# Kernel tuning notes

Hardware: AMD Instinct MI355X
Metric: run time of the kernel (lower is better)

## Reference

```python
import jax, jax.numpy as jnp
import numpy as np


def setup_inputs() -> dict:
    key = jax.random.key(0)
    k1, k2, k3, k4 = jax.random.split(key, 4)
    B, L, D = 16, 2048, 128
    return {
        "query": jax.random.normal(k1, (B, L, D), dtype=jnp.float32),
        "key": jax.random.normal(k2, (B, L, D), dtype=jnp.float32),
        "value": jax.random.normal(k3, (B, L, D), dtype=jnp.float32),
        "mask": jax.random.randint(k4, (B, L, L), 0, 2, dtype=jnp.int32),
    }


def reference(query, key, value, mask):
    # scores: [B, L_q, L_k], scaled by sqrt(D_q)
    scale = 1.0 / jnp.sqrt(jnp.asarray(query.shape[-1], dtype=query.dtype))
    scores = jnp.einsum("bqd,bkd->bqk", query, key) * scale
    NEG = jnp.asarray(-1e9, dtype=scores.dtype)
    scores = jnp.where(mask == 0, NEG, scores)
    p_attn = jax.nn.softmax(scores, axis=-1)
    context = jnp.einsum("bqk,bkd->bqd", p_attn, value)
    return (context, p_attn)
```

## Files before the change

kernel.cpp:

```cpp
#include <hip/hip_runtime.h>
#include <hip/hip_bf16.h>
#include <hip/hip_fp16.h>

#define BB 16
#define LL 2048
#define DD 128
#define SCALE 0.08838834764831845f
#define CEXP 12.0f
#define NT 32

typedef _Float16 f16x8 __attribute__((ext_vector_type(8)));
typedef float f32x16 __attribute__((ext_vector_type(16)));

#define MFMA32(a,b,c) __builtin_amdgcn_mfma_f32_32x32x16_f16((a),(b),(c),0,0,0)

#define OFF_KB   0
#define OFF_VB   65536
#define OFF_PB   131072
#define OFF_RED  147456
#define LDS_MAIN 148480

#define WAITVM(N)  asm volatile("s_waitcnt vmcnt(" #N ")" ::: "memory")
#define MEMFENCE   asm volatile("" ::: "memory")
#define SB0        __builtin_amdgcn_sched_barrier(0)

__device__ __forceinline__ f16x8 as_f16x8(uint4 v){
  union { uint4 u; f16x8 h; } x; x.u = v; return x.h;
}
__device__ __forceinline__ unsigned pkf16(float a, float b){
  __half ha = __float2half_rn(a), hb = __float2half_rn(b);
  return (unsigned)__half_as_ushort(ha) | ((unsigned)__half_as_ushort(hb) << 16);
}
__device__ __forceinline__ unsigned pkrtz(float a, float b){
  union { decltype(__builtin_amdgcn_cvt_pkrtz(0.f, 0.f)) h; unsigned u; } x;
  x.h = __builtin_amdgcn_cvt_pkrtz(a, b);
  return x.u;
}
__device__ __forceinline__ void stage16(const unsigned char* g, char* l){
  __builtin_amdgcn_global_load_lds(
      (const __attribute__((address_space(1))) void*)g,
      (__attribute__((address_space(3))) void*)l, 16, 0, 0);
}
__device__ __forceinline__ void stage2(const unsigned char* g, char* l, int soff){
  stage16(g + soff, l + soff);
  stage16(g + soff + 1024, l + soff + 1024);
}

__global__ __launch_bounds__(256) void prep_img(
    const float* __restrict__ K, const float* __restrict__ V,
    unsigned char* __restrict__ kimg, unsigned char* __restrict__ vimg)
{
  __shared__ float t[32][65];
  const int bid = blockIdx.x, tid = threadIdx.x;
  if (bid < 2048) {
    const int G = bid*256 + tid;
    const int b = G >> 15;
    const int k = (G >> 4) & 2047;
    const int gd = G & 15;
    const float* src = K + ((size_t)b*LL + k)*DD + gd*8;
    float4 f0 = *(const float4*)(src);
    float4 f1 = *(const float4*)(src + 4);
    uint4 o;
    o.x = pkf16(f0.x, f0.y); o.y = pkf16(f0.z, f0.w);
    o.z = pkf16(f1.x, f1.y); o.w = pkf16(f1.z, f1.w);
    const size_t base = ((size_t)b*NT + (k>>6))*16384;
    *(uint4*)(kimg + base + (k&63)*256 + ((gd*16) ^ ((k&15)<<4))) = o;
  } else {
    const int t2 = bid - 2048;
    const int b = t2 >> 7;
    const int rem = t2 & 127;
    const int kt = rem >> 2, dt = rem & 3;
    const int k0 = kt*64, d0 = dt*32;
    const int kl = tid >> 2, dq = (tid & 3)*8;
    const float* src = V + ((size_t)b*LL + k0 + kl)*DD + d0 + dq;
    float4 f0 = *(const float4*)(src);
    float4 f1 = *(const float4*)(src + 4);
    t[dq+0][kl] = f0.x; t[dq+1][kl] = f0.y; t[dq+2][kl] = f0.z; t[dq+3][kl] = f0.w;
    t[dq+4][kl] = f1.x; t[dq+5][kl] = f1.y; t[dq+6][kl] = f1.z; t[dq+7][kl] = f1.w;
    __syncthreads();
    const int dl = tid >> 3, kg = tid & 7;
    const int d = d0 + dl;
    uint4 o;
    o.x = pkf16(t[dl][kg*8+0], t[dl][kg*8+1]);
    o.y = pkf16(t[dl][kg*8+2], t[dl][kg*8+3]);
    o.z = pkf16(t[dl][kg*8+4], t[dl][kg*8+5]);
    o.w = pkf16(t[dl][kg*8+6], t[dl][kg*8+7]);
    const size_t base = ((size_t)b*NT + kt)*16384;
    *(uint4*)(vimg + base + d*128 + ((kg*16) ^ ((d&7)<<4))) = o;
  }
}

#define QKCOMPUTE(BUFIDX) \
  const char* kb = KB + (BUFIDX)*16384 + krow*256; \
  f32x16 aA, aB; \
  _Pragma("unroll") for (int i=0;i<16;++i){aA[i]=0.f;aB[i]=0.f;} \
  _Pragma("unroll") for (int s=0;s<4;++s){ \
    uint4 af = *(const uint4*)(kb + (((s*2+hi)*16) ^ kswz)); \
    aA = MFMA32(as_f16x8(af), as_f16x8(qf[s]), aA); } \
  _Pragma("unroll") for (int s=4;s<8;++s){ \
    uint4 af = *(const uint4*)(kb + (((s*2+hi)*16) ^ kswz)); \
    aB = MFMA32(as_f16x8(af), as_f16x8(qf[s]), aB); }

#define P1BODY(RR, WN) do { \
  WAITVM(WN); \
  __builtin_amdgcn_s_barrier(); \
  MEMFENCE; \
  int4 t0, t1, t2, t3; \
  { const int* mp2 = Mrow + (((RR)+2)&31)*64 + moff; \
    t0 = *(const int4*)(mp2);    t1 = *(const int4*)(mp2+8); \
    t2 = *(const int4*)(mp2+16); t3 = *(const int4*)(mp2+24); } \
  SB0; \
  stage2(KIMG + imgb + (size_t)(((RR)+3)&31)*16384, KB + (((RR)+3)&3)*16384, soff); \
  SB0; \
  QKCOMPUTE((RR)&3); \
  const unsigned w16 = (cm0.x?0x1u:0u) | (cm0.y?0x2u:0u) | (cm0.z?0x4u:0u) | (cm0.w?0x8u:0u) \
                     | (cm1.x?0x100u:0u) | (cm1.y?0x200u:0u) | (cm1.z?0x400u:0u) | (cm1.w?0x800u:0u) \
                     | (cm2.x?0x10000u:0u) | (cm2.y?0x20000u:0u) | (cm2.z?0x40000u:0u) | (cm2.w?0x80000u:0u) \
                     | (cm3.x?0x1000000u:0u) | (cm3.y?0x2000000u:0u) | (cm3.z?0x4000000u:0u) | (cm3.w?0x8000000u:0u); \
  { const unsigned pw = __shfl_xor(w16, 32); \
    if (l < 32) BMst[(RR)*2] = w16 | (pw << 4); } \
  _Pragma("unroll") for (int i=0;i<16;++i){ \
    const float sv = ((w16>>((i&3)+8*(i>>2)))&1u) ? fmaf(aA[i]+aB[i], SCALE, -CEXP) : -1.0e9f; \
    psum[i&3] += __expf(sv); } \
  cm0=n10; cm1=n11; cm2=n12; cm3=n13; \
  n10=t0; n11=t1; n12=t2; n13=t3; \
} while(0)

#define P2BODY(RR, NTOK) do { \
  WAITVM(NTOK); \
  __builtin_amdgcn_s_barrier(); \
  MEMFENCE; \
  const unsigned bn2 = BMl[2*(((RR)+2)&31)]; \
  SB0; \
  stage2(KIMG + imgb + (size_t)(((RR)+3)&31)*16384, KB + (((RR)+3)&3)*16384, soff); \
  stage2(VIMG + imgb + (size_t)(((RR)+3)&31)*16384, VB + (((RR)+3)&3)*16384, soff); \
  SB0; \
  QKCOMPUTE((RR)&3); \
  const unsigned bwh = bcur >> (4*hi); \
  float pv[16]; \
  _Pragma("unroll") for (int i=0;i<16;++i){ \
    const float sv = ((bwh>>((i&3)+8*(i>>2)))&1u) ? fmaf(aA[i]+aB[i], SCALE, -CEXP) : -1.0e9f; \
    pv[i] = __expf(sv) * inv; } \
  { float* pr = Prow + (size_t)(RR)*64 + sub*32 + hi*4; \
    float4 o; \
    o.x=pv[0];  o.y=pv[1];  o.z=pv[2];  o.w=pv[3];  *(float4*)(pr)    = o; \
    o.x=pv[4];  o.y=pv[5];  o.z=pv[6];  o.w=pv[7];  *(float4*)(pr+8)  = o; \
    o.x=pv[8];  o.y=pv[9];  o.z=pv[10]; o.w=pv[11]; *(float4*)(pr+16) = o; \
    o.x=pv[12]; o.y=pv[13]; o.z=pv[14]; o.w=pv[15]; *(float4*)(pr+24) = o; } \
  SB0; \
  { char* pb = PB + p*4096 + sub*2048; \
    uint2 u; \
    u.x = pkrtz(pv[0],pv[1]);   u.y = pkrtz(pv[2],pv[3]);   *(uint2*)(pb + c*16 + hi*8) = u; \
    u.x = pkrtz(pv[4],pv[5]);   u.y = pkrtz(pv[6],pv[7]);   *(uint2*)(pb + (c+32)*16 + hi*8) = u; \
    u.x = pkrtz(pv[8],pv[9]);   u.y = pkrtz(pv[10],pv[11]); *(uint2*)(pb + 1024 + c*16 + hi*8) = u; \
    u.x = pkrtz(pv[12],pv[13]); u.y = pkrtz(pv[14],pv[15]); *(uint2*)(pb + 1024 + (c+32)*16 + hi*8) = u; } \
  asm volatile("s_waitcnt lgkmcnt(0)" ::: "memory"); \
  __builtin_amdgcn_s_barrier(); \
  MEMFENCE; \
  _Pragma("unroll") for (int s2=0;s2<2;++s2){ \
    _Pragma("unroll") for (int k2=0;k2<2;++k2){ \
      const uint4 afr = *(const uint4*)(PB + p*4096 + s2*2048 + k2*1024 + l*16); \
      const int gix = s2*4 + k2*2 + hi; \
      const int d0v = sub*64 + c; \
      const uint4 b0 = *(const uint4*)(VB + ((RR)&3)*16384 + d0v*128 + ((gix*16) ^ ((d0v&7)<<4))); \
      ctx0 = MFMA32(as_f16x8(afr), as_f16x8(b0), ctx0); \
      const int d1v = sub*64 + 32 + c; \
      const uint4 b1 = *(const uint4*)(VB + ((RR)&3)*16384 + d1v*128 + ((gix*16) ^ ((d1v&7)<<4))); \
      ctx1 = MFMA32(as_f16x8(afr), as_f16x8(b1), ctx1); } } \
  bcur = bn1; bn1 = bn2; \
} while(0)

__global__ __launch_bounds__(512) void attn_main(
    const float* __restrict__ Q, const int* __restrict__ M,
    unsigned int* __restrict__ BM,
    const unsigned char* __restrict__ KIMG, const unsigned char* __restrict__ VIMG,
    float* __restrict__ ctxout, float* __restrict__ pout)
{
  extern __shared__ char lds[];
  char* KB = lds + OFF_KB;
  char* VB = lds + OFF_VB;
  char* PB = lds + OFF_PB;
  float* RED = (float*)(lds + OFF_RED);

  const int tid = threadIdx.x;
  const int w = tid >> 6, l = tid & 63;
  const int c = l & 31, hi = l >> 5;
  const int p = w >> 1, sub = w & 1;

  const int bid = blockIdx.x;
  const int xcd = bid & 7, jj = bid >> 3;
  const int b = xcd*2 + (jj >> 4);
  const int q0 = (jj & 15) * 128;
  const int qrow = q0 + p*32 + c;

  uint4 qf[8];
  const float* qp0 = Q + ((size_t)b*LL + qrow)*DD;
#pragma unroll
  for (int s = 0; s < 8; ++s) {
    const float4 f0 = *(const float4*)(qp0 + s*16 + hi*8);
    const float4 f1 = *(const float4*)(qp0 + s*16 + hi*8 + 4);
    uint4 qv;
    qv.x = pkf16(f0.x, f0.y); qv.y = pkf16(f0.z, f0.w);
    qv.z = pkf16(f1.x, f1.y); qv.w = pkf16(f1.z, f1.w);
    qf[s] = qv;
  }

  const size_t imgb = ((size_t)b * NT) * 16384;
  const int soff = w*2048 + l*16;
  const int* Mrow = M + ((size_t)b*LL + qrow)*LL;
  const int moff = sub*32 + hi*4;
  unsigned int* BMst = BM + ((size_t)b*LL + qrow)*64 + sub;
  const unsigned int* BMl = BMst;
  const int krow = sub*32 + c;
  const int kswz = (c & 15) << 4;

  int4 cm0, cm1, cm2, cm3, n10, n11, n12, n13;
  stage2(KIMG + imgb + 0*16384, KB + 0*16384, soff); SB0;
  { const int* mp = Mrow + moff;
    cm0 = *(const int4*)(mp);    cm1 = *(const int4*)(mp+8);
    cm2 = *(const int4*)(mp+16); cm3 = *(const int4*)(mp+24); } SB0;
  stage2(KIMG + imgb + 1*16384, KB + 1*16384, soff); SB0;
  { const int* mp = Mrow + 64 + moff;
    n10 = *(const int4*)(mp);    n11 = *(const int4*)(mp+8);
    n12 = *(const int4*)(mp+16); n13 = *(const int4*)(mp+24); } SB0;
  stage2(KIMG + imgb + 2*16384, KB + 2*16384, soff); SB0;

  float psum[4] = {0.f, 0.f, 0.f, 0.f};
  P1BODY(0, 8);
  P1BODY(1, 9);
#pragma unroll 1
  for (int r = 2; r < 32; ++r) {
    P1BODY(r, 10);
  }
  float sum = (psum[0] + psum[1]) + (psum[2] + psum[3]);
  sum += __shfl_xor(sum, 32);
  __syncthreads();
  if (l < 32) RED[(p*2+sub)*32 + c] = sum;
  __syncthreads();
  float tot = RED[(p*2+sub)*32 + c] + RED[(p*2+(1-sub))*32 + c];
  tot = fmaxf(tot, 1e-35f);
  const float inv = 1.0f / tot;
  __syncthreads();

  stage2(KIMG + imgb + 0*16384, KB + 0*16384, soff);
  stage2(VIMG + imgb + 0*16384, VB + 0*16384, soff); SB0;
  unsigned bcur = BMl[0]; SB0;
  stage2(KIMG + imgb + 1*16384, KB + 1*16384, soff);
  stage2(VIMG + imgb + 1*16384, VB + 1*16384, soff); SB0;
  unsigned bn1 = BMl[2]; SB0;
  stage2(KIMG + imgb + 2*16384, KB + 2*16384, soff);
  stage2(VIMG + imgb + 2*16384, VB + 2*16384, soff); SB0;

  f32x16 ctx0, ctx1;
#pragma unroll
  for (int i = 0; i < 16; ++i) { ctx0[i] = 0.f; ctx1[i] = 0.f; }
  float* Prow = pout + ((size_t)b*LL + qrow)*LL;

  P2BODY(0, 10);
  P2BODY(1, 14);
  P2BODY(2, 18);
#pragma unroll 1
  for (int r = 3; r < 32; ++r) {
    P2BODY(r, 22);
  }

#pragma unroll
  for (int reg = 0; reg < 16; ++reg) {
    const int q = q0 + p*32 + (reg&3) + 8*(reg>>2) + 4*hi;
    float* cr = ctxout + ((size_t)b*LL + q)*DD;
    cr[sub*64 + c]      = ctx0[reg];
    cr[sub*64 + 32 + c] = ctx1[reg];
  }
}

__global__ __launch_bounds__(256) void attn_naive(
    const float* __restrict__ Q, const float* __restrict__ K,
    const float* __restrict__ V, const int* __restrict__ M,
    float* __restrict__ ctx, float* __restrict__ pout)
{
  const int b = blockIdx.x >> 11;
  const int q = blockIdx.x & (LL-1);
  __shared__ float s[LL];
  __shared__ float red[256];
  const int tid = threadIdx.x;
  const float* qp = Q + ((size_t)b*LL + q)*DD;
  for (int kk = tid; kk < LL; kk += 256) {
    const float* kp = K + ((size_t)b*LL + kk)*DD;
    float a = 0.f;
    for (int d = 0; d < DD; ++d) a += qp[d]*kp[d];
    s[kk] = M[((size_t)b*LL + q)*LL + kk] ? a*SCALE : -1e9f;
  }
  __syncthreads();
  float mx = -3e38f;
  for (int kk = tid; kk < LL; kk += 256) mx = fmaxf(mx, s[kk]);
  red[tid] = mx; __syncthreads();
  for (int o = 128; o >= 1; o >>= 1) {
    if (tid < o) red[tid] = fmaxf(red[tid], red[tid+o]);
    __syncthreads();
  }
  const float mrow = red[0]; __syncthreads();
  float sm = 0.f;
  for (int kk = tid; kk < LL; kk += 256) { float e = __expf(s[kk]-mrow); s[kk] = e; sm += e; }
  red[tid] = sm; __syncthreads();
  for (int o = 128; o >= 1; o >>= 1) {
    if (tid < o) red[tid] += red[tid+o];
    __syncthreads();
  }
  const float inv = 1.0f / red[0]; __syncthreads();
  float* prow = pout + ((size_t)b*LL + q)*LL;
  for (int kk = tid; kk < LL; kk += 256) { s[kk] *= inv; prow[kk] = s[kk]; }
  __syncthreads();
  if (tid < DD) {
    float a = 0.f;
    for (int kk = 0; kk < LL; ++kk) a += s[kk]*V[((size_t)b*LL + kk)*DD + tid];
    ctx[((size_t)b*LL + q)*DD + tid] = a;
  }
}

extern "C" void kernel_launch(void* const* d_in, const int* in_sizes, int n_in,
                              void* d_out, int out_size, void* d_ws, size_t ws_size,
                              hipStream_t stream) {
  (void)in_sizes; (void)n_in; (void)out_size;
  const float* Q = (const float*)d_in[0];
  const float* K = (const float*)d_in[1];
  const float* V = (const float*)d_in[2];
  const int*   M = (const int*)d_in[3];
  float* ctx  = (float*)d_out;
  float* pout = ctx + (size_t)BB*LL*DD;
  const size_t IMG = (size_t)BB*NT*16384;
  const size_t NBM = (size_t)BB*LL*(LL/32);
  const size_t WS_NEED = IMG*2 + NBM*4;
  if (ws_size >= WS_NEED) {
    unsigned char* kimg = (unsigned char*)d_ws;
    unsigned char* vimg = kimg + IMG;
    unsigned int*  bmw  = (unsigned int*)(vimg + IMG);
    hipFuncSetAttribute(reinterpret_cast<const void*>(attn_main),
                        hipFuncAttributeMaxDynamicSharedMemorySize, LDS_MAIN);
    prep_img<<<4096, 256, 0, stream>>>(K, V, kimg, vimg);
    attn_main<<<256, 512, LDS_MAIN, stream>>>(Q, M, bmw, kimg, vimg, ctx, pout);
  } else {
    attn_naive<<<BB*LL, 256, 0, stream>>>(Q, K, V, M, ctx, pout);
  }
}
```

Measured before the change: 218.2 us.

## Stage mask tiles into LDS via async global_load_lds with swizzled layout

Pass 1 no longer loads mask int4s directly into registers two steps ahead. Each block now cooperatively stages 128x64 mask tiles into a double-buffered LDS region with async direct-to-LDS loads and an XOR swizzle, then reads them back from LDS. The aim is coalesced, fully-line mask reads, lower register pressure, and a simpler vmcnt pipeline. The cost is more LDS traffic. The mask buffer also reuses the V buffer region, so phase 1 must finish with it before phase 2 stages V.

```diff
diff --git a/kernel.cpp b/kernel.cpp
--- a/kernel.cpp
+++ b/kernel.cpp
@@ -15,10 +15,11 @@
 #define MFMA32(a,b,c) __builtin_amdgcn_mfma_f32_32x32x16_f16((a),(b),(c),0,0,0)
 
 #define OFF_KB   0
-#define OFF_VB   65536
+#define OFF_MB   65536
 #define OFF_PB   131072
 #define OFF_RED  147456
 #define LDS_MAIN 148480
+#define OFF_VB   65536
 
 #define WAITVM(N)  asm volatile("s_waitcnt vmcnt(" #N ")" ::: "memory")
 #define MEMFENCE   asm volatile("" ::: "memory")
@@ -44,6 +45,12 @@
 __device__ __forceinline__ void stage2(const unsigned char* g, char* l, int soff){
   stage16(g + soff, l + soff);
   stage16(g + soff + 1024, l + soff + 1024);
+}
+__device__ __forceinline__ void mstage(const unsigned char* msrc, char* mdst, int roff){
+  stage16(msrc + roff,          mdst);
+  stage16(msrc + roff + 262144, mdst + 8192);
+  stage16(msrc + roff + 524288, mdst + 16384);
+  stage16(msrc + roff + 786432, mdst + 24576);
 }
 
 __global__ __launch_bounds__(256) void prep_img(
@@ -105,32 +112,32 @@
   WAITVM(WN); \
   __builtin_amdgcn_s_barrier(); \
   MEMFENCE; \
-  int4 t0, t1, t2, t3; \
-  { const int* mp2 = Mrow + (((RR)+2)&31)*64 + moff; \
-    t0 = *(const int4*)(mp2);    t1 = *(const int4*)(mp2+8); \
-    t2 = *(const int4*)(mp2+16); t3 = *(const int4*)(mp2+24); } \
+  mstage(msrc, mdw + (((RR)+1)&1)*32768, (((RR)+1)&31)*256); \
   SB0; \
   stage2(KIMG + imgb + (size_t)(((RR)+3)&31)*16384, KB + (((RR)+3)&3)*16384, soff); \
   SB0; \
   QKCOMPUTE((RR)&3); \
-  const unsigned w16 = (cm0.x?0x1u:0u) | (cm0.y?0x2u:0u) | (cm0.z?0x4u:0u) | (cm0.w?0x8u:0u) \
-                     | (cm1.x?0x100u:0u) | (cm1.y?0x200u:0u) | (cm1.z?0x400u:0u) | (cm1.w?0x800u:0u) \
-                     | (cm2.x?0x10000u:0u) | (cm2.y?0x20000u:0u) | (cm2.z?0x40000u:0u) | (cm2.w?0x80000u:0u) \
-                     | (cm3.x?0x1000000u:0u) | (cm3.y?0x2000000u:0u) | (cm3.z?0x4000000u:0u) | (cm3.w?0x8000000u:0u); \
+  const char* mb = mrd + ((RR)&1)*32768; \
+  const int4 m0 = *(const int4*)(mb + mo0); \
+  const int4 m1 = *(const int4*)(mb + mo1); \
+  const int4 m2 = *(const int4*)(mb + mo2); \
+  const int4 m3 = *(const int4*)(mb + mo3); \
+  const unsigned w16 = (m0.x?0x1u:0u)|(m0.y?0x2u:0u)|(m0.z?0x4u:0u)|(m0.w?0x8u:0u) \
+                     | (m1.x?0x100u:0u)|(m1.y?0x200u:0u)|(m1.z?0x400u:0u)|(m1.w?0x800u:0u) \
+                     | (m2.x?0x10000u:0u)|(m2.y?0x20000u:0u)|(m2.z?0x40000u:0u)|(m2.w?0x80000u:0u) \
+                     | (m3.x?0x1000000u:0u)|(m3.y?0x2000000u:0u)|(m3.z?0x4000000u:0u)|(m3.w?0x8000000u:0u); \
   { const unsigned pw = __shfl_xor(w16, 32); \
-    if (l < 32) BMst[(RR)*2] = w16 | (pw << 4); } \
+    if (l < 32) BM[bmbase + (RR)*2] = w16 | (pw << 4); } \
   _Pragma("unroll") for (int i=0;i<16;++i){ \
     const float sv = ((w16>>((i&3)+8*(i>>2)))&1u) ? fmaf(aA[i]+aB[i], SCALE, -CEXP) : -1.0e9f; \
     psum[i&3] += __expf(sv); } \
-  cm0=n10; cm1=n11; cm2=n12; cm3=n13; \
-  n10=t0; n11=t1; n12=t2; n13=t3; \
 } while(0)
 
 #define P2BODY(RR, NTOK) do { \
   WAITVM(NTOK); \
   __builtin_amdgcn_s_barrier(); \
   MEMFENCE; \
-  const unsigned bn2 = BMl[2*(((RR)+2)&31)]; \
+  const unsigned bn2 = BM[bmbase + 2*(((RR)+2)&31)]; \
   SB0; \
   stage2(KIMG + imgb + (size_t)(((RR)+3)&31)*16384, KB + (((RR)+3)&3)*16384, soff); \
   stage2(VIMG + imgb + (size_t)(((RR)+3)&31)*16384, VB + (((RR)+3)&3)*16384, soff); \
@@ -207,30 +214,31 @@
 
   const size_t imgb = ((size_t)b * NT) * 16384;
   const int soff = w*2048 + l*16;
-  const int* Mrow = M + ((size_t)b*LL + qrow)*LL;
-  const int moff = sub*32 + hi*4;
-  unsigned int* BMst = BM + ((size_t)b*LL + qrow)*64 + sub;
-  const unsigned int* BMl = BMst;
+  const size_t bmbase = ((size_t)b*LL + qrow)*64 + sub;
   const int krow = sub*32 + c;
   const int kswz = (c & 15) << 4;
 
-  int4 cm0, cm1, cm2, cm3, n10, n11, n12, n13;
+  const int srow = w*4 + (l >> 4);
+  const unsigned char* msrc = (const unsigned char*)M
+      + ((size_t)(b*LL + q0 + srow))*LL*4 + (size_t)(((l & 15) ^ (srow & 15)) * 16);
+  char* mdw = lds + OFF_MB + w*1024 + l*16;
+  const int rowc = p*32 + c;
+  const char* mrd = lds + OFF_MB + rowc*256;
+  const int mswz = rowc & 15;
+  const int cbx = sub*8 + hi;
+  const int mo0 = ((cbx+0)^mswz)*16, mo1 = ((cbx+2)^mswz)*16;
+  const int mo2 = ((cbx+4)^mswz)*16, mo3 = ((cbx+6)^mswz)*16;
+
   stage2(KIMG + imgb + 0*16384, KB + 0*16384, soff); SB0;
-  { const int* mp = Mrow + moff;
-    cm0 = *(const int4*)(mp);    cm1 = *(const int4*)(mp+8);
-    cm2 = *(const int4*)(mp+16); cm3 = *(const int4*)(mp+24); } SB0;
+  mstage(msrc, mdw + 0*32768, 0*256); SB0;
   stage2(KIMG + imgb + 1*16384, KB + 1*16384, soff); SB0;
-  { const int* mp = Mrow + 64 + moff;
-    n10 = *(const int4*)(mp);    n11 = *(const int4*)(mp+8);
-    n12 = *(const int4*)(mp+16); n13 = *(const int4*)(mp+24); } SB0;
   stage2(KIMG + imgb + 2*16384, KB + 2*16384, soff); SB0;
 
   float psum[4] = {0.f, 0.f, 0.f, 0.f};
-  P1BODY(0, 8);
-  P1BODY(1, 9);
+  P1BODY(0, 4);
 #pragma unroll 1
-  for (int r = 2; r < 32; ++r) {
-    P1BODY(r, 10);
+  for (int r = 1; r < 32; ++r) {
+    P1BODY(r, 3);
   }
   float sum = (psum[0] + psum[1]) + (psum[2] + psum[3]);
   sum += __shfl_xor(sum, 32);
@@ -244,10 +252,10 @@
 
   stage2(KIMG + imgb + 0*16384, KB + 0*16384, soff);
   stage2(VIMG + imgb + 0*16384, VB + 0*16384, soff); SB0;
-  unsigned bcur = BMl[0]; SB0;
+  unsigned bcur = BM[bmbase]; SB0;
   stage2(KIMG + imgb + 1*16384, KB + 1*16384, soff);
   stage2(VIMG + imgb + 1*16384, VB + 1*16384, soff); SB0;
-  unsigned bn1 = BMl[2]; SB0;
+  unsigned bn1 = BM[bmbase + 2]; SB0;
   stage2(KIMG + imgb + 2*16384, KB + 2*16384, soff);
   stage2(VIMG + imgb + 2*16384, VB + 2*16384, soff); SB0;
 
```

Result: no change. 216.8 us (-0.7%).
